# Kernel tuning notes

Measured on AMD Instinct MI355X. Metric: run time of the kernel, lower is better.

## Reference

```python
import jax, jax.numpy as jnp
import numpy as np

LABEL_NUM = 32      # distinct identities in the batch
K = 16              # samples per class per modality
MODALITIES = 3      # feats is chunked into label_num*3 groups
M = LABEL_NUM * K * MODALITIES   # 1536 total samples
N = LABEL_NUM * MODALITIES       # 96 centers (one per chunk)
STRIPES = 8         # local horizontal stripes
D_LOCAL = 1024      # per-stripe local feature dim
FEAT_DIM = STRIPES * D_LOCAL     # 8192 global feature dim
MARGIN = 0.3


def setup_inputs() -> dict:
    key = jax.random.key(0)
    k1, k2 = jax.random.split(key)
    feats = jax.random.normal(k1, (M, FEAT_DIM), dtype=jnp.float32)
    # chunk-structured labels: each contiguous block of K samples shares a label,
    # pattern repeated for each of the 3 modality streams
    labels = jnp.tile(jnp.repeat(jnp.arange(LABEL_NUM, dtype=jnp.int32), K), MODALITIES)
    local_features = jax.random.normal(k2, (M, D_LOCAL, STRIPES), dtype=jnp.float32)
    return {"feats": feats, "labels": labels, "local_features": local_features}


def _pdist(a, b):
    # euclidean distance matrix [m, n] (matches pdist_torch incl. 1e-12 clamp)
    d2 = (jnp.sum(a * a, axis=1)[:, None]
          + jnp.sum(b * b, axis=1)[None, :]
          - 2.0 * (a @ b.T))
    return jnp.sqrt(jnp.clip(d2, 1e-12, None))


def _batch_euclidean_dist(x, y):
    # x: [B, m, d], y: [B, n, d] -> [B, m, n]
    d2 = (jnp.sum(x * x, axis=-1)[:, :, None]
          + jnp.sum(y * y, axis=-1)[:, None, :]
          - 2.0 * jnp.einsum('bmd,bnd->bmn', x, y))
    return jnp.sqrt(jnp.clip(d2, 1e-12, None))


def _shortest_dist(d):
    # d: [B, m, n]; AlignedReID shortest-path DP over the (m, n) grid -> [B]
    mm, nn = d.shape[1], d.shape[2]
    dp = [[None] * nn for _ in range(mm)]
    for i in range(mm):
        for j in range(nn):
            if i == 0 and j == 0:
                dp[i][j] = d[:, i, j]
            elif i == 0:
                dp[i][j] = dp[i][j - 1] + d[:, i, j]
            elif j == 0:
                dp[i][j] = dp[i - 1][j] + d[:, i, j]
            else:
                dp[i][j] = jnp.minimum(dp[i - 1][j], dp[i][j - 1]) + d[:, i, j]
    return dp[-1][-1]


def _batch_local_dist(x, y):
    d = _batch_euclidean_dist(x, y)
    d = (jnp.exp(d) - 1.0) / (jnp.exp(d) + 1.0)  # normalize to (0, 1)
    return _shortest_dist(d)


def reference(feats, labels, local_features):
    m = feats.shape[0]          # 1536
    n = N                       # 96 chunks/centers
    k = m // n                  # 16 samples per chunk
    # per-chunk centers (mean over each contiguous chunk of feats)
    centers = feats.reshape(n, k, -1).mean(axis=1)          # [N, D]
    dist = _pdist(centers, feats)                           # [N, M]
    anchor_labels = labels[::k]                             # label of each chunk, [N]
    is_pos = anchor_labels[:, None] == labels[None, :]      # [N, M]
    masked_pos = jnp.where(is_pos, dist, -jnp.inf)
    p_inds = jnp.argmax(masked_pos, axis=1)                 # hardest positive per center
    masked_neg = jnp.where(is_pos, jnp.inf, dist)
    n_inds = jnp.argmin(masked_neg, axis=1)                 # hardest negative per center
    lf = jnp.transpose(local_features, (0, 2, 1))           # [M, stripes, d_local]
    p_local = lf[p_inds]                                    # [N, stripes, d_local]
    n_local = lf[n_inds]
    inputs1 = centers.reshape(n, STRIPES, -1)               # [N, stripes, d_local]
    local_dist_ap = _batch_local_dist(inputs1, p_local)     # [N]
    local_dist_an = _batch_local_dist(inputs1, n_local)     # [N]
    # MarginRankingLoss(x1=an, x2=ap, y=1): mean(relu(ap - an + margin))
    loss = jnp.mean(jax.nn.relu(local_dist_ap - local_dist_an + MARGIN))
    return loss
```

## Files before the change

kernel.cpp:

```cpp
#include <hip/hip_runtime.h>
#include <math.h>

#define M_ROWS 1536
#define NC 96
#define KG 16
#define FD 8192
#define NS 8
#define MARGIN 0.3f

#define KSPLIT 32
#define KCH 256
#define BKS 32
#define NST (KCH / BKS)
#define BN 64

typedef short v8s __attribute__((ext_vector_type(8)));
typedef float v4f __attribute__((ext_vector_type(4)));

__device__ __forceinline__ void split4t(float4 v, ushort4* h, ushort4* l) {
    const unsigned int ux = __float_as_uint(v.x), uy = __float_as_uint(v.y);
    const unsigned int uz = __float_as_uint(v.z), uw = __float_as_uint(v.w);
    *h = make_ushort4((unsigned short)(ux >> 16), (unsigned short)(uy >> 16),
                      (unsigned short)(uz >> 16), (unsigned short)(uw >> 16));
    const float rx = v.x - __uint_as_float(ux & 0xffff0000u);
    const float ry = v.y - __uint_as_float(uy & 0xffff0000u);
    const float rz = v.z - __uint_as_float(uz & 0xffff0000u);
    const float rw = v.w - __uint_as_float(uw & 0xffff0000u);
    *l = make_ushort4((unsigned short)(__float_as_uint(rx) >> 16),
                      (unsigned short)(__float_as_uint(ry) >> 16),
                      (unsigned short)(__float_as_uint(rz) >> 16),
                      (unsigned short)(__float_as_uint(rw) >> 16));
}

__global__ void centers_kernel(const float* __restrict__ feats,
                               float* __restrict__ centers,
                               float* __restrict__ fnp,
                               float* __restrict__ cnp) {
    const int c = blockIdx.x;
    const int bd = blockIdx.y;
    const int tid = threadIdx.x;

    float sq[KG];
#pragma unroll
    for (int k = 0; k < KG; ++k) sq[k] = 0.f;
    float cp = 0.f;

#pragma unroll
    for (int it = 0; it < 2; ++it) {
        const int base = bd * 2048 + it * 1024 + tid * 4;
        float4 acc = make_float4(0.f, 0.f, 0.f, 0.f);
#pragma unroll
        for (int k = 0; k < KG; ++k) {
            const float4 v = *(const float4*)&feats[(size_t)(c * KG + k) * FD + base];
            acc.x += v.x; acc.y += v.y; acc.z += v.z; acc.w += v.w;
            sq[k] += v.x * v.x + v.y * v.y + v.z * v.z + v.w * v.w;
        }
        float4 cv = make_float4(acc.x * 0.0625f, acc.y * 0.0625f,
                                acc.z * 0.0625f, acc.w * 0.0625f);
        *(float4*)&centers[(size_t)c * FD + base] = cv;
        cp += cv.x * cv.x + cv.y * cv.y + cv.z * cv.z + cv.w * cv.w;
    }

    const int lane = tid & 63;
    const int w = tid >> 6;
    __shared__ float wred[4][17];
#pragma unroll
    for (int k = 0; k < KG; ++k) {
        float v = sq[k];
#pragma unroll
        for (int off = 32; off > 0; off >>= 1) v += __shfl_down(v, off, 64);
        if (lane == 0) wred[w][k] = v;
    }
    {
        float v = cp;
#pragma unroll
        for (int off = 32; off > 0; off >>= 1) v += __shfl_down(v, off, 64);
        if (lane == 0) wred[w][16] = v;
    }
    __syncthreads();
    if (tid < 17) {
        const float t = wred[0][tid] + wred[1][tid] + wred[2][tid] + wred[3][tid];
        if (tid < 16) fnp[bd * M_ROWS + c * KG + tid] = t;
        else          cnp[bd * NC + c] = t;
    }
}

__global__ __launch_bounds__(256) void gemm11_kernel(const float* __restrict__ centers,
                                                     const float* __restrict__ feats,
                                                     float* __restrict__ part) {
    const int bid = blockIdx.x;
    const int ks = bid & 31;
    const int nb = bid >> 5;
    const int tid = threadIdx.x;
    const int j0 = nb * BN;
    const int k0b = ks * KCH;

    __shared__ unsigned short AH[2][6 * 512], AL[2][6 * 512];
    __shared__ unsigned short BH[2][4 * 512], BL[2][4 * 512];

    int aoff[3], aidx[3];
#pragma unroll
    for (int i = 0; i < 3; ++i) {
        const int q = tid + i * 256;
        const int m = q >> 3, kk = (q & 7) * 4;
        aoff[i] = m * FD + kk;
        aidx[i] = (m >> 4) * 512 + ((m & 15) | ((kk >> 3) << 4)) * 8 + (kk & 7);
    }
    int boff[2], bidx[2];
#pragma unroll
    for (int i = 0; i < 2; ++i) {
        const int q = tid + i * 256;
        const int n = q >> 3, kk = (q & 7) * 4;
        boff[i] = (j0 + n) * FD + kk;
        bidx[i] = (n >> 4) * 512 + ((n & 15) | ((kk >> 3) << 4)) * 8 + (kk & 7);
    }

    float4 pa[3], pb[2];
#pragma unroll
    for (int i = 0; i < 3; ++i) pa[i] = *(const float4*)&centers[aoff[i] + k0b];
#pragma unroll
    for (int i = 0; i < 2; ++i) pb[i] = *(const float4*)&feats[boff[i] + k0b];
#pragma unroll
    for (int i = 0; i < 3; ++i) {
        ushort4 h, l; split4t(pa[i], &h, &l);
        *(ushort4*)&AH[0][aidx[i]] = h; *(ushort4*)&AL[0][aidx[i]] = l;
    }
#pragma unroll
    for (int i = 0; i < 2; ++i) {
        ushort4 h, l; split4t(pb[i], &h, &l);
        *(ushort4*)&BH[0][bidx[i]] = h; *(ushort4*)&BL[0][bidx[i]] = l;
    }
    __syncthreads();

    v4f acc[3][2];
#pragma unroll
    for (int a = 0; a < 3; ++a)
#pragma unroll
        for (int b = 0; b < 2; ++b) {
            acc[a][b][0] = 0.f; acc[a][b][1] = 0.f;
            acc[a][b][2] = 0.f; acc[a][b][3] = 0.f;
        }

    const int w = tid >> 6, lane = tid & 63;
    const int wm = w >> 1, wn = w & 1;
    const int fo = lane * 8;

    int cur = 0;
    for (int st = 0; st < NST; ++st) {
        if (st < NST - 1) {
            const int k0 = k0b + (st + 1) * BKS;
#pragma unroll
            for (int i = 0; i < 3; ++i) pa[i] = *(const float4*)&centers[aoff[i] + k0];
#pragma unroll
            for (int i = 0; i < 2; ++i) pb[i] = *(const float4*)&feats[boff[i] + k0];
        }

        v8s Bhf[2], Blf[2];
#pragma unroll
        for (int nt = 0; nt < 2; ++nt) {
            Bhf[nt] = *(const v8s*)&BH[cur][(wn * 2 + nt) * 512 + fo];
            Blf[nt] = *(const v8s*)&BL[cur][(wn * 2 + nt) * 512 + fo];
        }
#pragma unroll
        for (int mt = 0; mt < 3; ++mt) {
            const v8s Ahf = *(const v8s*)&AH[cur][(wm * 3 + mt) * 512 + fo];
            const v8s Alf = *(const v8s*)&AL[cur][(wm * 3 + mt) * 512 + fo];
#pragma unroll
            for (int nt = 0; nt < 2; ++nt) {
                acc[mt][nt] = __builtin_amdgcn_mfma_f32_16x16x32_bf16(Ahf, Bhf[nt], acc[mt][nt], 0, 0, 0);
                acc[mt][nt] = __builtin_amdgcn_mfma_f32_16x16x32_bf16(Ahf, Blf[nt], acc[mt][nt], 0, 0, 0);
                acc[mt][nt] = __builtin_amdgcn_mfma_f32_16x16x32_bf16(Alf, Bhf[nt], acc[mt][nt], 0, 0, 0);
            }
        }

        if (st < NST - 1) {
            const int d = cur ^ 1;
#pragma unroll
            for (int i = 0; i < 3; ++i) {
                ushort4 h, l; split4t(pa[i], &h, &l);
                *(ushort4*)&AH[d][aidx[i]] = h; *(ushort4*)&AL[d][aidx[i]] = l;
            }
#pragma unroll
            for (int i = 0; i < 2; ++i) {
                ushort4 h, l; split4t(pb[i], &h, &l);
                *(ushort4*)&BH[d][bidx[i]] = h; *(ushort4*)&BL[d][bidx[i]] = l;
            }
        }
        __syncthreads();
        cur ^= 1;
    }

    const int col = lane & 15, r0 = (lane >> 4) * 4;
#pragma unroll
    for (int mt = 0; mt < 3; ++mt) {
#pragma unroll
        for (int nt = 0; nt < 2; ++nt) {
            const int n = j0 + (wn * 2 + nt) * 16 + col;
#pragma unroll
            for (int j = 0; j < 4; ++j) {
                const int m = (wm * 3 + mt) * 16 + r0 + j;
                part[((size_t)m * KSPLIT + ks) * M_ROWS + n] = acc[mt][nt][j];
            }
        }
    }
}

__global__ void select_kernel(const float* __restrict__ part,
                              const float* __restrict__ fnp,
                              const float* __restrict__ cnp,
                              const int* __restrict__ labels,
                              int* __restrict__ pinds,
                              int* __restrict__ ninds) {
    const int c = blockIdx.x;
    const int tid = threadIdx.x;
    const int anchor = labels[c * KG];

    float cn = 0.f;
#pragma unroll
    for (int b = 0; b < 4; ++b) cn += cnp[b * NC + c];

    float bestp = -INFINITY; int bpi = 1 << 30;
    float bestn =  INFINITY; int bni = 1 << 30;

    const float* pc = part + (size_t)c * KSPLIT * M_ROWS;
    for (int j = tid; j < M_ROWS; j += 256) {
        float dot = 0.f;
#pragma unroll
        for (int p = 0; p < KSPLIT; ++p)
            dot += pc[(size_t)p * M_ROWS + j];
        float fn = 0.f;
#pragma unroll
        for (int b = 0; b < 4; ++b) fn += fnp[b * M_ROWS + j];
        const float d2 = cn + fn - 2.f * dot;
        const bool pos = (labels[j] == anchor);
        if (pos) {
            if (d2 > bestp || (d2 == bestp && j < bpi)) { bestp = d2; bpi = j; }
        } else {
            if (d2 < bestn || (d2 == bestn && j < bni)) { bestn = d2; bni = j; }
        }
    }

    __shared__ float sv[256];
    __shared__ int   si[256];
    sv[tid] = bestp; si[tid] = bpi; __syncthreads();
    for (int s = 128; s > 0; s >>= 1) {
        if (tid < s) {
            if (sv[tid + s] > sv[tid] ||
                (sv[tid + s] == sv[tid] && si[tid + s] < si[tid])) {
                sv[tid] = sv[tid + s]; si[tid] = si[tid + s];
            }
        }
        __syncthreads();
    }
    if (tid == 0) pinds[c] = si[0];
    __syncthreads();
    sv[tid] = bestn; si[tid] = bni; __syncthreads();
    for (int s = 128; s > 0; s >>= 1) {
        if (tid < s) {
            if (sv[tid + s] < sv[tid] ||
                (sv[tid + s] == sv[tid] && si[tid + s] < si[tid])) {
                sv[tid] = sv[tid + s]; si[tid] = si[tid + s];
            }
        }
        __syncthreads();
    }
    if (tid == 0) ninds[c] = si[0];
}

__global__ void local_kernel(const float* __restrict__ centers,
                             const float* __restrict__ localf,
                             const int* __restrict__ pinds,
                             const int* __restrict__ ninds,
                             float* __restrict__ res) {
    const int c = blockIdx.x;
    const int which = blockIdx.y;
    const int tid = threadIdx.x;
    const int idx = (which == 0) ? pinds[c] : ninds[c];

    __shared__ float xl[NS * 1028];
    __shared__ float yl[NS * 1032];
    __shared__ float sred[256];
    __shared__ float dmat[64];
    __shared__ float xx[8], yy[8], xyv[64];

#pragma unroll
    for (int it = 0; it < 8; ++it) {
        const int q = tid + it * 256;
        const float4 v = *(const float4*)&centers[(size_t)c * FD + q * 4];
        const int i = q >> 8;
        const int d = (q * 4) & 1023;
        *(float4*)&xl[i * 1028 + d] = v;

        const float4 w = *(const float4*)&localf[(size_t)idx * FD + q * 4];
        const int jb = (q * 4) & 7;
        const int dd = q >> 1;
        yl[(jb + 0) * 1032 + dd] = w.x;
        yl[(jb + 1) * 1032 + dd] = w.y;
        yl[(jb + 2) * 1032 + dd] = w.z;
        yl[(jb + 3) * 1032 + dd] = w.w;
    }
    __syncthreads();

    const int p = tid >> 2, c4 = tid & 3;
    const int i = p >> 3, j = p & 7;
    float s = 0.f;
    for (int t = 0; t < 64; ++t) {
        const int d = c4 * 4 + t * 16;
        const float4 xv = *(const float4*)&xl[i * 1028 + d];
        const float4 yv = *(const float4*)&yl[j * 1032 + d];
        s += xv.x * yv.x + xv.y * yv.y + xv.z * yv.z + xv.w * yv.w;
    }
    sred[tid] = s;
    __syncthreads();
    if (tid < 64)
        xyv[tid] = sred[tid * 4] + sred[tid * 4 + 1] + sred[tid * 4 + 2] + sred[tid * 4 + 3];

    float s2 = 0.f;
    if (tid < 64) {
        const int r = tid >> 2;
        const float* base = (r < 8) ? &xl[r * 1028] : &yl[(r - 8) * 1032];
        for (int t = 0; t < 64; ++t) {
            const int d = c4 * 4 + t * 16;
            const float4 v = *(const float4*)&base[d];
            s2 += v.x * v.x + v.y * v.y + v.z * v.z + v.w * v.w;
        }
    }
    __syncthreads();
    sred[tid] = s2;
    __syncthreads();
    if (tid < 16) {
        const float v = sred[tid * 4] + sred[tid * 4 + 1] + sred[tid * 4 + 2] + sred[tid * 4 + 3];
        if (tid < 8) xx[tid] = v; else yy[tid - 8] = v;
    }
    __syncthreads();

    if (tid < 64) {
        const float d2 = xx[i] + yy[j] - 2.f * xyv[tid];
        const float d = sqrtf(fmaxf(d2, 1e-12f));
        dmat[tid] = tanhf(0.5f * d);
    }
    __syncthreads();

    if (tid == 0) {
        float prev[8], cur[8];
        cur[0] = dmat[0];
#pragma unroll
        for (int jj = 1; jj < 8; ++jj) cur[jj] = cur[jj - 1] + dmat[jj];
        for (int ii = 1; ii < 8; ++ii) {
#pragma unroll
            for (int jj = 0; jj < 8; ++jj) prev[jj] = cur[jj];
            cur[0] = prev[0] + dmat[ii * 8];
#pragma unroll
            for (int jj = 1; jj < 8; ++jj)
                cur[jj] = fminf(prev[jj], cur[jj - 1]) + dmat[ii * 8 + jj];
        }
        res[which * NC + c] = cur[7];
    }
}

__global__ void loss_kernel(const float* __restrict__ res, float* __restrict__ out) {
    const int tid = threadIdx.x;
    float v = 0.f;
    if (tid < NC) v = fmaxf(res[tid] - res[NC + tid] + MARGIN, 0.f);
#pragma unroll
    for (int off = 32; off > 0; off >>= 1) v += __shfl_down(v, off, 64);
    __shared__ float w2[2];
    const int lane = tid & 63, w = tid >> 6;
    if (lane == 0) w2[w] = v;
    __syncthreads();
    if (tid == 0) out[0] = (w2[0] + w2[1]) * (1.f / NC);
}

extern "C" void kernel_launch(void* const* d_in, const int* in_sizes, int n_in,
                              void* d_out, int out_size, void* d_ws, size_t ws_size,
                              hipStream_t stream) {
    const float* feats  = (const float*)d_in[0];
    const int*   labels = (const int*)d_in[1];
    const float* localf = (const float*)d_in[2];
    float* out = (float*)d_out;

    float* centers = (float*)d_ws;
    float* part    = centers + (size_t)NC * FD;
    float* fnp     = part + (size_t)NC * KSPLIT * M_ROWS;
    float* cnp     = fnp + 4 * M_ROWS;
    float* res     = cnp + 4 * NC;
    int*   pinds   = (int*)(res + 2 * NC);
    int*   ninds   = pinds + NC;

    hipLaunchKernelGGL(centers_kernel, dim3(NC, 4), dim3(256), 0, stream,
                       feats, centers, fnp, cnp);
    hipLaunchKernelGGL(gemm11_kernel, dim3(24 * KSPLIT), dim3(256), 0, stream,
                       centers, feats, part);
    hipLaunchKernelGGL(select_kernel, dim3(NC), dim3(256), 0, stream,
                       part, fnp, cnp, labels, pinds, ninds);
    hipLaunchKernelGGL(local_kernel, dim3(NC, 2), dim3(256), 0, stream,
                       centers, localf, pinds, ninds, res);
    hipLaunchKernelGGL(loss_kernel, dim3(1), dim3(128), 0, stream, res, out);
}
```

Measured before the change: 52.54 us.

## Pre-split centers to bf16 hi/lo, async LDS loads, fuse loss into local kernel

```diff
diff --git a/kernel.cpp b/kernel.cpp
--- a/kernel.cpp
+++ b/kernel.cpp
@@ -32,8 +32,16 @@
                       (unsigned short)(__float_as_uint(rw) >> 16));
 }
 
+__device__ __forceinline__ void gload16u(const unsigned short* g, unsigned short* lds) {
+    __builtin_amdgcn_global_load_lds(
+        (const __attribute__((address_space(1))) void*)g,
+        (__attribute__((address_space(3))) void*)lds, 16, 0, 0);
+}
+
 __global__ void centers_kernel(const float* __restrict__ feats,
                                float* __restrict__ centers,
+                               unsigned short* __restrict__ ch,
+                               unsigned short* __restrict__ cl,
                                float* __restrict__ fnp,
                                float* __restrict__ cnp) {
     const int c = blockIdx.x;
@@ -58,6 +66,9 @@
         float4 cv = make_float4(acc.x * 0.0625f, acc.y * 0.0625f,
                                 acc.z * 0.0625f, acc.w * 0.0625f);
         *(float4*)&centers[(size_t)c * FD + base] = cv;
+        ushort4 h, l; split4t(cv, &h, &l);
+        *(ushort4*)&ch[(size_t)c * FD + base] = h;
+        *(ushort4*)&cl[(size_t)c * FD + base] = l;
         cp += cv.x * cv.x + cv.y * cv.y + cv.z * cv.z + cv.w * cv.w;
     }
 
@@ -85,7 +96,8 @@
     }
 }
 
-__global__ __launch_bounds__(256) void gemm11_kernel(const float* __restrict__ centers,
+__global__ __launch_bounds__(256) void gemm14_kernel(const unsigned short* __restrict__ ch,
+                                                     const unsigned short* __restrict__ cl,
                                                      const float* __restrict__ feats,
                                                      float* __restrict__ part) {
     const int bid = blockIdx.x;
@@ -95,16 +107,19 @@
     const int j0 = nb * BN;
     const int k0b = ks * KCH;
 
-    __shared__ unsigned short AH[2][6 * 512], AL[2][6 * 512];
+    __shared__ unsigned short AHL[2][12 * 512];
     __shared__ unsigned short BH[2][4 * 512], BL[2][4 * 512];
 
-    int aoff[3], aidx[3];
+    const unsigned short* asrc[3];
+    int albase[3];
 #pragma unroll
     for (int i = 0; i < 3; ++i) {
-        const int q = tid + i * 256;
-        const int m = q >> 3, kk = (q & 7) * 4;
-        aoff[i] = m * FD + kk;
-        aidx[i] = (m >> 4) * 512 + ((m & 15) | ((kk >> 3) << 4)) * 8 + (kk & 7);
+        const int cchunk = tid + i * 256;
+        const int t = cchunk >> 6, l = cchunk & 63;
+        const int mt = t >> 1;
+        const unsigned short* basep = (t & 1) ? cl : ch;
+        asrc[i] = basep + (size_t)(mt * 16 + (l & 15)) * FD + (l >> 4) * 8;
+        albase[i] = (i * 256 + (tid & 192)) * 8;
     }
     int boff[2], bidx[2];
 #pragma unroll
@@ -115,16 +130,11 @@
         bidx[i] = (n >> 4) * 512 + ((n & 15) | ((kk >> 3) << 4)) * 8 + (kk & 7);
     }
 
-    float4 pa[3], pb[2];
-#pragma unroll
-    for (int i = 0; i < 3; ++i) pa[i] = *(const float4*)&centers[aoff[i] + k0b];
+    float4 pb[2];
+#pragma unroll
+    for (int i = 0; i < 3; ++i) gload16u(asrc[i] + k0b, &AHL[0][albase[i]]);
 #pragma unroll
     for (int i = 0; i < 2; ++i) pb[i] = *(const float4*)&feats[boff[i] + k0b];
-#pragma unroll
-    for (int i = 0; i < 3; ++i) {
-        ushort4 h, l; split4t(pa[i], &h, &l);
-        *(ushort4*)&AH[0][aidx[i]] = h; *(ushort4*)&AL[0][aidx[i]] = l;
-    }
 #pragma unroll
     for (int i = 0; i < 2; ++i) {
         ushort4 h, l; split4t(pb[i], &h, &l);
@@ -150,7 +160,7 @@
         if (st < NST - 1) {
             const int k0 = k0b + (st + 1) * BKS;
 #pragma unroll
-            for (int i = 0; i < 3; ++i) pa[i] = *(const float4*)&centers[aoff[i] + k0];
+            for (int i = 0; i < 3; ++i) gload16u(asrc[i] + k0, &AHL[cur ^ 1][albase[i]]);
 #pragma unroll
             for (int i = 0; i < 2; ++i) pb[i] = *(const float4*)&feats[boff[i] + k0];
         }
@@ -163,8 +173,9 @@
         }
 #pragma unroll
         for (int mt = 0; mt < 3; ++mt) {
-            const v8s Ahf = *(const v8s*)&AH[cur][(wm * 3 + mt) * 512 + fo];
-            const v8s Alf = *(const v8s*)&AL[cur][(wm * 3 + mt) * 512 + fo];
+            const int M = wm * 3 + mt;
+            const v8s Ahf = *(const v8s*)&AHL[cur][(2 * M) * 512 + fo];
+            const v8s Alf = *(const v8s*)&AHL[cur][(2 * M + 1) * 512 + fo];
 #pragma unroll
             for (int nt = 0; nt < 2; ++nt) {
                 acc[mt][nt] = __builtin_amdgcn_mfma_f32_16x16x32_bf16(Ahf, Bhf[nt], acc[mt][nt], 0, 0, 0);
@@ -176,11 +187,6 @@
         if (st < NST - 1) {
             const int d = cur ^ 1;
 #pragma unroll
-            for (int i = 0; i < 3; ++i) {
-                ushort4 h, l; split4t(pa[i], &h, &l);
-                *(ushort4*)&AH[d][aidx[i]] = h; *(ushort4*)&AL[d][aidx[i]] = l;
-            }
-#pragma unroll
             for (int i = 0; i < 2; ++i) {
                 ushort4 h, l; split4t(pb[i], &h, &l);
                 *(ushort4*)&BH[d][bidx[i]] = h; *(ushort4*)&BL[d][bidx[i]] = l;
@@ -205,12 +211,12 @@
     }
 }
 
-__global__ void select_kernel(const float* __restrict__ part,
-                              const float* __restrict__ fnp,
-                              const float* __restrict__ cnp,
-                              const int* __restrict__ labels,
-                              int* __restrict__ pinds,
-                              int* __restrict__ ninds) {
+__global__ __launch_bounds__(512) void select_kernel(const float* __restrict__ part,
+                                                     const float* __restrict__ fnp,
+                                                     const float* __restrict__ cnp,
+                                                     const int* __restrict__ labels,
+                                                     int* __restrict__ pinds,
+                                                     int* __restrict__ ninds) {
     const int c = blockIdx.x;
     const int tid = threadIdx.x;
     const int anchor = labels[c * KG];
@@ -223,7 +229,7 @@
     float bestn =  INFINITY; int bni = 1 << 30;
 
     const float* pc = part + (size_t)c * KSPLIT * M_ROWS;
-    for (int j = tid; j < M_ROWS; j += 256) {
+    for (int j = tid; j < M_ROWS; j += 512) {
         float dot = 0.f;
 #pragma unroll
         for (int p = 0; p < KSPLIT; ++p)
@@ -240,10 +246,10 @@
         }
     }
 
-    __shared__ float sv[256];
-    __shared__ int   si[256];
+    __shared__ float sv[512];
+    __shared__ int   si[512];
     sv[tid] = bestp; si[tid] = bpi; __syncthreads();
-    for (int s = 128; s > 0; s >>= 1) {
+    for (int s = 256; s > 0; s >>= 1) {
         if (tid < s) {
             if (sv[tid + s] > sv[tid] ||
                 (sv[tid + s] == sv[tid] && si[tid + s] < si[tid])) {
@@ -255,7 +261,7 @@
     if (tid == 0) pinds[c] = si[0];
     __syncthreads();
     sv[tid] = bestn; si[tid] = bni; __syncthreads();
-    for (int s = 128; s > 0; s >>= 1) {
+    for (int s = 256; s > 0; s >>= 1) {
         if (tid < s) {
             if (sv[tid + s] < sv[tid] ||
                 (sv[tid + s] == sv[tid] && si[tid + s] < si[tid])) {
@@ -271,7 +277,9 @@
                              const float* __restrict__ localf,
                              const int* __restrict__ pinds,
                              const int* __restrict__ ninds,
-                             float* __restrict__ res) {
+                             float* __restrict__ res,
+                             int* __restrict__ counter,
+                             float* __restrict__ out) {
     const int c = blockIdx.x;
     const int which = blockIdx.y;
     const int tid = threadIdx.x;
@@ -282,6 +290,7 @@
     __shared__ float sred[256];
     __shared__ float dmat[64];
     __shared__ float xx[8], yy[8], xyv[64];
+    __shared__ int lastFlag;
 
 #pragma unroll
     for (int it = 0; it < 8; ++it) {
@@ -355,20 +364,24 @@
                 cur[jj] = fminf(prev[jj], cur[jj - 1]) + dmat[ii * 8 + jj];
         }
         res[which * NC + c] = cur[7];
-    }
-}
-
-__global__ void loss_kernel(const float* __restrict__ res, float* __restrict__ out) {
-    const int tid = threadIdx.x;
-    float v = 0.f;
-    if (tid < NC) v = fmaxf(res[tid] - res[NC + tid] + MARGIN, 0.f);
-#pragma unroll
-    for (int off = 32; off > 0; off >>= 1) v += __shfl_down(v, off, 64);
-    __shared__ float w2[2];
-    const int lane = tid & 63, w = tid >> 6;
-    if (lane == 0) w2[w] = v;
-    __syncthreads();
-    if (tid == 0) out[0] = (w2[0] + w2[1]) * (1.f / NC);
+        __threadfence();
+        const int old = atomicAdd(counter, 1);
+        lastFlag = (old == 2 * NC - 1);
+    }
+    __syncthreads();
+
+    if (lastFlag) {
+        __threadfence();
+        float v = 0.f;
+        if (tid < NC) v = fmaxf(res[tid] - res[NC + tid] + MARGIN, 0.f);
+#pragma unroll
+        for (int off = 32; off > 0; off >>= 1) v += __shfl_down(v, off, 64);
+        __shared__ float w4[4];
+        const int lane = tid & 63, wv = tid >> 6;
+        if (lane == 0) w4[wv] = v;
+        __syncthreads();
+        if (tid == 0) out[0] = (w4[0] + w4[1]) * (1.f / NC);
+    }
 }
 
 extern "C" void kernel_launch(void* const* d_in, const int* in_sizes, int n_in,
@@ -384,16 +397,19 @@
     float* fnp     = part + (size_t)NC * KSPLIT * M_ROWS;
     float* cnp     = fnp + 4 * M_ROWS;
     float* res     = cnp + 4 * NC;
-    int*   pinds   = (int*)(res + 2 * NC);
+    unsigned short* ch = (unsigned short*)(res + 2 * NC);
+    unsigned short* cl = ch + (size_t)NC * FD;
+    int*   pinds   = (int*)(cl + (size_t)NC * FD);
     int*   ninds   = pinds + NC;
-
+    int*   counter = ninds + NC;
+
+    hipMemsetAsync(counter, 0, sizeof(int), stream);
     hipLaunchKernelGGL(centers_kernel, dim3(NC, 4), dim3(256), 0, stream,
-                       feats, centers, fnp, cnp);
-    hipLaunchKernelGGL(gemm11_kernel, dim3(24 * KSPLIT), dim3(256), 0, stream,
-                       centers, feats, part);
-    hipLaunchKernelGGL(select_kernel, dim3(NC), dim3(256), 0, stream,
+                       feats, centers, ch, cl, fnp, cnp);
+    hipLaunchKernelGGL(gemm14_kernel, dim3(24 * KSPLIT), dim3(256), 0, stream,
+                       ch, cl, feats, part);
+    hipLaunchKernelGGL(select_kernel, dim3(NC), dim3(512), 0, stream,
                        part, fnp, cnp, labels, pinds, ninds);
     hipLaunchKernelGGL(local_kernel, dim3(NC, 2), dim3(256), 0, stream,
-                       centers, localf, pinds, ninds, res);
-    hipLaunchKernelGGL(loss_kernel, dim3(1), dim3(128), 0, stream, res, out);
-}
+                       centers, localf, pinds, ninds, res, counter, out);
+}
```

After: 64.25 us. 1.22x slower.
